# Performance work log

Hardware: AMD Instinct MI355X
Metric: run time of the kernel (lower is better)

Reference implementation:

```python
import jax, jax.numpy as jnp
import numpy as np

EPS = 1e-6
N_SRC = 100000
N_TAR = 100000
N = N_SRC + N_TAR
DIM = 128
E = 600000
NEG_SLOPE = 0.01  # torch leaky_relu default


def setup_inputs() -> dict:
    key = jax.random.key(0)
    ks = jax.random.split(key, 8)
    x_src = jax.random.normal(ks[0], (N_SRC, DIM), dtype=jnp.float32)
    x_tar = jax.random.normal(ks[1], (N_TAR, DIM), dtype=jnp.float32)
    edge_index = jax.random.randint(ks[2], (2, E), 0, N, dtype=jnp.int64)
    edge_weight = jax.random.uniform(ks[3], (E,), dtype=jnp.float32)
    W_gcn = jax.random.normal(ks[4], (DIM, DIM), dtype=jnp.float32) / np.sqrt(DIM)
    b_gcn = jax.random.normal(ks[5], (DIM,), dtype=jnp.float32) * 0.01
    W_fnn = jax.random.normal(ks[6], (DIM, DIM), dtype=jnp.float32) / np.sqrt(DIM)
    b_fnn = jax.random.normal(ks[7], (DIM,), dtype=jnp.float32) * 0.01
    return dict(x_src=x_src, x_tar=x_tar, edge_index=edge_index,
                edge_weight=edge_weight, W_gcn=W_gcn, b_gcn=b_gcn,
                W_fnn=W_fnn, b_fnn=b_fnn)


def _gcn_conv(x, edge_index, edge_weight, W, b):
    # PyG GCNConv with add_self_loops=True, symmetric normalization.
    row = jnp.concatenate([edge_index[0], jnp.arange(N, dtype=edge_index.dtype)])
    col = jnp.concatenate([edge_index[1], jnp.arange(N, dtype=edge_index.dtype)])
    w = jnp.concatenate([edge_weight, jnp.ones((N,), dtype=edge_weight.dtype)])
    deg = jax.ops.segment_sum(w, col, num_segments=N)
    dinv = jnp.where(deg > 0, jax.lax.rsqrt(deg), 0.0)
    norm = dinv[row] * w * dinv[col]                 # [E+N]
    h = x @ W                                        # [N, D]
    msg = norm[:, None] * h[row]                     # gather + scale
    out = jnp.zeros_like(h).at[col].add(msg)         # scatter-add to targets
    return out + b


def _node_norm(x):
    mean = jnp.mean(x, axis=1, keepdims=True)
    var = jnp.mean((x - mean) ** 2, axis=1, keepdims=True)  # unbiased=False
    return (x - mean) / jnp.sqrt(var + EPS)


def reference(x_src, x_tar, edge_index, edge_weight, W_gcn, b_gcn, W_fnn, b_fnn):
    x = jnp.concatenate([x_src, x_tar], axis=0)      # [N, D]
    # route == 'MIX': GNN branch + FNN branch on the skip copy
    g = _gcn_conv(x, edge_index, edge_weight, W_gcn, b_gcn)
    f = jax.nn.leaky_relu(x @ W_fnn + b_fnn, NEG_SLOPE)  # dropout = identity (eval)
    x = g + f
    x = _node_norm(x)
    x = jax.nn.leaky_relu(x, NEG_SLOPE)
    return x[:N_SRC, :], x[N_SRC:, :]
```

## Files before the change

### kernel.cpp

```cpp
#include <hip/hip_runtime.h>
#include <hip/hip_bf16.h>
#include <cstddef>
#include <cstdint>

#define DIM 128
#define SCAN_CHUNK 2048

typedef __attribute__((ext_vector_type(8))) short short8v;
typedef __attribute__((ext_vector_type(4))) float f32x4;

__device__ __forceinline__ float leaky(float v) {
    return v > 0.0f ? v : 0.01f * v;
}

__device__ __forceinline__ unsigned short f2bf(float f) {
    unsigned u = __builtin_bit_cast(unsigned, f);
    u += 0x7FFF + ((u >> 16) & 1);
    return (unsigned short)(u >> 16);
}

__device__ __forceinline__ unsigned cvt_pk_bf16(float a, float b) {
    unsigned r;
    asm("v_cvt_pk_bf16_f32 %0, %1, %2" : "=v"(r) : "v"(a), "v"(b));
    return r;
}

__device__ __forceinline__ float bf2f_hi(unsigned p) {
    return __builtin_bit_cast(float, p & 0xFFFF0000u);
}
__device__ __forceinline__ float bf2f_lo(unsigned p) {
    return __builtin_bit_cast(float, p << 16);
}

__device__ __forceinline__ void gload_lds16(const float* g, float* lds) {
    __builtin_amdgcn_global_load_lds(
        (const __attribute__((address_space(1))) unsigned int*)g,
        (__attribute__((address_space(3))) unsigned int*)lds, 16, 0, 0);
}

__global__ __launch_bounds__(256)
void hist_kernel(const int* __restrict__ col, int* __restrict__ cnt, int E,
                 const float* __restrict__ Wg, const float* __restrict__ Wf,
                 unsigned short* __restrict__ WgT, unsigned short* __restrict__ WfT) {
    int gid = blockIdx.x * blockDim.x + threadIdx.x;
    if (gid < 128 * 128) {
        int c = gid >> 7, k = gid & 127;
        WgT[c * 128 + k] = f2bf(Wg[k * 128 + c]);
        WfT[c * 128 + k] = f2bf(Wf[k * 128 + c]);
    }
    if (gid < E) atomicAdd(&cnt[col[gid]], 1);
}

__global__ __launch_bounds__(256)
void scan_block_sums(const int* __restrict__ cnt, int* __restrict__ bsum, int N) {
    __shared__ int sdata[4];
    int base = blockIdx.x * SCAN_CHUNK;
    int s = 0;
    for (int k = threadIdx.x; k < SCAN_CHUNK; k += 256) {
        int idx = base + k;
        s += (idx < N) ? cnt[idx] : 0;
    }
#pragma unroll
    for (int m = 1; m < 64; m <<= 1) s += __shfl_xor(s, m, 64);
    if ((threadIdx.x & 63) == 0) sdata[threadIdx.x >> 6] = s;
    __syncthreads();
    if (threadIdx.x == 0)
        bsum[blockIdx.x] = sdata[0] + sdata[1] + sdata[2] + sdata[3];
}

__global__ __launch_bounds__(128)
void scan_bsum_kernel(int* __restrict__ bsum, int nb) {
    __shared__ int wtot[2];
    int t = threadIdx.x;
    int lane = t & 63;
    int orig = (t < nb) ? bsum[t] : 0;
    int v = orig;
#pragma unroll
    for (int m = 1; m < 64; m <<= 1) {
        int u = __shfl_up(v, m, 64);
        if (lane >= m) v += u;
    }
    if (lane == 63) wtot[t >> 6] = v;
    __syncthreads();
    if (t >= 64) v += wtot[0];
    if (t < nb) bsum[t] = v - orig;
}

__global__ __launch_bounds__(256)
void scan_write_kernel(int* __restrict__ cnt, const int* __restrict__ bsum,
                       int* __restrict__ off, int N) {
    __shared__ int wsum[4];
    int t = threadIdx.x;
    int base = blockIdx.x * SCAN_CHUNK + t * 8;
    int vals[8];
    int local = 0;
#pragma unroll
    for (int k = 0; k < 8; ++k) {
        int idx = base + k;
        int c = (idx < N) ? cnt[idx] : 0;
        vals[k] = local;
        local += c;
    }
    int tsum = local;
    int lane = t & 63;
    int v = tsum;
#pragma unroll
    for (int m = 1; m < 64; m <<= 1) {
        int u = __shfl_up(v, m, 64);
        if (lane >= m) v += u;
    }
    if (lane == 63) wsum[t >> 6] = v;
    __syncthreads();
    int woff = 0;
    for (int i = 0; i < (t >> 6); ++i) woff += wsum[i];
    int texcl = (v - tsum) + woff + bsum[blockIdx.x];
#pragma unroll
    for (int k = 0; k < 8; ++k) {
        int idx = base + k;
        int o = texcl + vals[k];
        if (idx <= N) off[idx] = o;
    }
    __syncthreads();
#pragma unroll
    for (int k = 0; k < 8; ++k) {
        int idx = base + k;
        int o = texcl + vals[k];
        if (idx < N) cnt[idx] = o;
    }
}

__global__ __launch_bounds__(256)
void reorder_kernel(const int* __restrict__ row, const int* __restrict__ col,
                    const float* __restrict__ w, int* __restrict__ cursor,
                    int2* __restrict__ edgeRW, int E) {
    int e = blockIdx.x * blockDim.x + threadIdx.x;
    if (e < E) {
        int c = col[e];
        int pos = atomicAdd(&cursor[c], 1);
        edgeRW[pos] = make_int2(row[e], __builtin_bit_cast(int, w[e]));
    }
}

__global__ __launch_bounds__(512, 4)
void gemm_mfma_kernel(const float* __restrict__ x_src, const float* __restrict__ x_tar,
                      int n_src, int n_total, int ntiles,
                      const int* __restrict__ off, const int2* __restrict__ edgeRW,
                      const unsigned short* __restrict__ WgT,
                      const unsigned short* __restrict__ WfT,
                      const float* __restrict__ bg, const float* __restrict__ bf,
                      unsigned short* __restrict__ hsb,
                      unsigned short* __restrict__ accb)
{
    __shared__ float Ash[4][32 * 128];
    __shared__ float dinvS[448];

    const int t    = threadIdx.x;
    const int lane = t & 63;
    const int wv   = t >> 6;
    const int h    = wv >> 2;
    const int q    = wv & 3;
    const int lr   = lane & 15;
    const int lk   = lane >> 4;

    const int nb  = gridDim.x;
    const int K   = (ntiles + nb - 1) / nb;
    const int t0  = blockIdx.x * K;
    const int cnt = min(K, ntiles - t0);
    if (cnt <= 0) return;

    for (int tt = t; tt < cnt * 32; tt += 512) {
        int gi = t0 * 32 + tt;
        if (gi >= n_total) gi = n_total - 1;
        int s0 = off[gi], e0 = off[gi + 1];
        float a = 1.0f;
        for (int j = s0; j < e0; ++j)
            a += __builtin_bit_cast(float, edgeRW[j].y);
        dinvS[tt] = rsqrtf(a);
    }
    asm volatile("s_waitcnt lgkmcnt(0)" ::: "memory");
    __builtin_amdgcn_sched_barrier(0);
    asm volatile("s_waitcnt vmcnt(0)" ::: "memory");
    __builtin_amdgcn_sched_barrier(0);

    short8v wg[4][2], wf[4][2];
#pragma unroll
    for (int ks = 0; ks < 4; ++ks)
#pragma unroll
        for (int nf = 0; nf < 2; ++nf) {
            int col = q * 32 + ((lr >> 2) << 3) + nf * 4 + (lr & 3);
            const size_t bo = (size_t)col * 128 + ks * 32 + lk * 8;
            wg[ks][nf] = *(const short8v*)(WgT + bo);
            wf[ks][nf] = *(const short8v*)(WfT + bo);
        }
    const int cb = q * 32 + lk * 8;
    float4 bgv[2], bfv[2];
#pragma unroll
    for (int nf = 0; nf < 2; ++nf) {
        bgv[nf] = *(const float4*)(bg + cb + nf * 4);
        bfv[nf] = *(const float4*)(bf + cb + nf * 4);
    }
    __builtin_amdgcn_sched_barrier(0);
    asm volatile("s_waitcnt vmcnt(0)" ::: "memory");
    __builtin_amdgcn_sched_barrier(0);

    auto stage = [&](int tl, int buf) {
#pragma unroll
        for (int s = 0; s < 2; ++s) {
            int id  = s * 512 + t;
            int row = id >> 5;
            int cs  = id & 31;
            int c   = cs ^ (row & 15);
            int rg  = tl * 32 + row;
            if (rg >= n_total) rg = n_total - 1;
            const float* xr = (rg < n_src) ? x_src + (size_t)rg * DIM
                                           : x_tar + (size_t)(rg - n_src) * DIM;
            gload_lds16(xr + c * 4, &Ash[buf][(size_t)(s * 512 + wv * 64) * 4]);
        }
    };

    stage(t0, 0);
    if (1 < cnt) stage(t0 + 1, 1);
    if (2 < cnt) stage(t0 + 2, 2);

    const int xrow = h * 16 + lr;
    const int xrs  = xrow & 15;

    for (int it = 0; it < cnt; ++it) {
        if (cnt >= 6) {
            if (it == 0)              asm volatile("s_waitcnt vmcnt(4)"  ::: "memory");
            else if (it == 1)         asm volatile("s_waitcnt vmcnt(6)"  ::: "memory");
            else if (it == 2)         asm volatile("s_waitcnt vmcnt(8)"  ::: "memory");
            else if (it == cnt - 2)   asm volatile("s_waitcnt vmcnt(8)"  ::: "memory");
            else if (it == cnt - 1)   asm volatile("s_waitcnt vmcnt(6)"  ::: "memory");
            else                      asm volatile("s_waitcnt vmcnt(10)" ::: "memory");
        } else {
            asm volatile("s_waitcnt vmcnt(0)" ::: "memory");
        }
        __builtin_amdgcn_sched_barrier(0);
        __builtin_amdgcn_s_barrier();
        __builtin_amdgcn_sched_barrier(0);

        if (it + 3 < cnt) stage(t0 + it + 3, (it + 3) & 3);

        const int cur = it & 3;
        f32x4 accg[2], accf[2];
        accg[0] = (f32x4)0.0f; accg[1] = (f32x4)0.0f;
        accf[0] = (f32x4)0.0f; accf[1] = (f32x4)0.0f;

#pragma unroll
        for (int ks = 0; ks < 4; ++ks) {
            int c0 = ks * 8 + lk * 2;
            float4 q0 = *(const float4*)&Ash[cur][(size_t)(xrow * 32 + ( c0      ^ xrs)) * 4];
            float4 q1 = *(const float4*)&Ash[cur][(size_t)(xrow * 32 + ((c0 + 1) ^ xrs)) * 4];
            union { short8v v; unsigned u[4]; } cv;
            cv.u[0] = cvt_pk_bf16(q0.x, q0.y);
            cv.u[1] = cvt_pk_bf16(q0.z, q0.w);
            cv.u[2] = cvt_pk_bf16(q1.x, q1.y);
            cv.u[3] = cvt_pk_bf16(q1.z, q1.w);
#pragma unroll
            for (int nf = 0; nf < 2; ++nf) {
                accg[nf] = __builtin_amdgcn_mfma_f32_16x16x32_bf16(wg[ks][nf], cv.v, accg[nf], 0, 0, 0);
                accf[nf] = __builtin_amdgcn_mfma_f32_16x16x32_bf16(wf[ks][nf], cv.v, accf[nf], 0, 0, 0);
            }
        }

        const int tile = t0 + it;
        int r = tile * 32 + xrow;
        const bool valid = (r < n_total);
        float dv = dinvS[it * 32 + xrow];

        float hs[8], oo[8];
#pragma unroll
        for (int nf = 0; nf < 2; ++nf)
#pragma unroll
            for (int e = 0; e < 4; ++e) {
                int k = nf * 4 + e;
                hs[k] = dv * accg[nf][e];
                float f = accf[nf][e] + ((const float*)&bfv[nf])[e];
                oo[k] = leaky(f) + ((const float*)&bgv[nf])[e] + dv * hs[k];
            }

        uint4 hp, op;
        hp.x = cvt_pk_bf16(hs[0], hs[1]); hp.y = cvt_pk_bf16(hs[2], hs[3]);
        hp.z = cvt_pk_bf16(hs[4], hs[5]); hp.w = cvt_pk_bf16(hs[6], hs[7]);
        op.x = cvt_pk_bf16(oo[0], oo[1]); op.y = cvt_pk_bf16(oo[2], oo[3]);
        op.z = cvt_pk_bf16(oo[4], oo[5]); op.w = cvt_pk_bf16(oo[6], oo[7]);

        if (valid) {
            *(uint4*)(hsb  + (size_t)r * DIM + cb) = hp;
            *(uint4*)(accb + (size_t)r * DIM + cb) = op;
        }
    }
}

__global__ __launch_bounds__(256)
void gather_norm_kernel(const int* __restrict__ off, const int2* __restrict__ edgeRW,
                        const unsigned short* __restrict__ hsb,
                        const unsigned short* __restrict__ accb,
                        float* __restrict__ out, int n)
{
    const int wid  = threadIdx.x >> 6;
    const int lane = threadIdx.x & 63;
    const int sub  = lane >> 4;
    const int sl   = lane & 15;
    int i = (blockIdx.x * 4 + wid) * 4 + sub;
    if (i >= n) i = n - 1;

    const int start = off[i];
    const int degc  = off[i + 1] - start;

    int md = degc;
    md = max(md, __shfl_xor(md, 16, 64));
    md = max(md, __shfl_xor(md, 32, 64));

    float s[8];
#pragma unroll
    for (int k = 0; k < 8; ++k) s[k] = 0.0f;
    float sw = 0.0f;

    const unsigned short* gbase = hsb + (size_t)sl * 8;

    int   r0 = 0, r1 = 0;
    float w0 = 0.0f, w1 = 0.0f;
    if (0 < degc) { int2 m = edgeRW[start];     r0 = m.x; w0 = __builtin_bit_cast(float, m.y); }
    if (1 < degc) { int2 m = edgeRW[start + 1]; r1 = m.x; w1 = __builtin_bit_cast(float, m.y); }
    uint4 p0 = *(const uint4*)(gbase + (size_t)r0 * DIM);

    for (int t = 0; t < md; ++t) {
        uint4 p1 = p0;
        if (t + 1 < md)
            p1 = *(const uint4*)(gbase + (size_t)r1 * DIM);
        int r2 = 0; float w2 = 0.0f;
        if (t + 2 < md) {
            if (t + 2 < degc) {
                int2 m = edgeRW[start + t + 2];
                r2 = m.x; w2 = __builtin_bit_cast(float, m.y);
            }
        }
        sw += w0;
        s[0] += w0 * bf2f_lo(p0.x); s[1] += w0 * bf2f_hi(p0.x);
        s[2] += w0 * bf2f_lo(p0.y); s[3] += w0 * bf2f_hi(p0.y);
        s[4] += w0 * bf2f_lo(p0.z); s[5] += w0 * bf2f_hi(p0.z);
        s[6] += w0 * bf2f_lo(p0.w); s[7] += w0 * bf2f_hi(p0.w);
        p0 = p1;
        r0 = r1; w0 = w1;
        r1 = r2; w1 = w2;
    }

    const float dv = rsqrtf(1.0f + sw);
    uint4 av = *(const uint4*)(accb + (size_t)i * DIM + sl * 8);
    float v[8];
    v[0] = bf2f_lo(av.x) + dv * s[0]; v[1] = bf2f_hi(av.x) + dv * s[1];
    v[2] = bf2f_lo(av.y) + dv * s[2]; v[3] = bf2f_hi(av.y) + dv * s[3];
    v[4] = bf2f_lo(av.z) + dv * s[4]; v[5] = bf2f_hi(av.z) + dv * s[5];
    v[6] = bf2f_lo(av.w) + dv * s[6]; v[7] = bf2f_hi(av.w) + dv * s[7];

    float sum = 0.0f;
#pragma unroll
    for (int k = 0; k < 8; ++k) sum += v[k];
#pragma unroll
    for (int m = 1; m < 16; m <<= 1) sum += __shfl_xor(sum, m, 64);
    const float mean = sum * (1.0f / 128.0f);

    float sq = 0.0f;
#pragma unroll
    for (int k = 0; k < 8; ++k) {
        v[k] -= mean;
        sq += v[k] * v[k];
    }
#pragma unroll
    for (int m = 1; m < 16; m <<= 1) sq += __shfl_xor(sq, m, 64);
    const float rstd = rsqrtf(sq * (1.0f / 128.0f) + 1e-6f);

    float4 o1, o2;
    o1.x = leaky(v[0] * rstd); o1.y = leaky(v[1] * rstd);
    o1.z = leaky(v[2] * rstd); o1.w = leaky(v[3] * rstd);
    o2.x = leaky(v[4] * rstd); o2.y = leaky(v[5] * rstd);
    o2.z = leaky(v[6] * rstd); o2.w = leaky(v[7] * rstd);
    float* op = out + (size_t)i * DIM + sl * 8;
    *(float4*)op       = o1;
    *(float4*)(op + 4) = o2;
}

extern "C" void kernel_launch(void* const* d_in, const int* in_sizes, int n_in,
                              void* d_out, int out_size, void* d_ws, size_t ws_size,
                              hipStream_t stream)
{
    const float* x_src = (const float*)d_in[0];
    const float* x_tar = (const float*)d_in[1];
    const int*   ei    = (const int*)d_in[2];
    const float* ew    = (const float*)d_in[3];
    const float* Wg    = (const float*)d_in[4];
    const float* bg    = (const float*)d_in[5];
    const float* Wf    = (const float*)d_in[6];
    const float* bf    = (const float*)d_in[7];

    const int n_src = in_sizes[0] / DIM;
    const int n_tar = in_sizes[1] / DIM;
    const int N     = n_src + n_tar;
    const int E     = in_sizes[3];

    const int* rowp = ei;
    const int* colp = ei + E;

    char* p = (char*)d_ws;
    int*   cnt  = (int*)p;    p += (size_t)N * 4;
    int*   off  = (int*)p;    p += (size_t)(N + 1) * 4;
    int*   bsum = (int*)p;    p += 160 * 4;
    p = (char*)(((uintptr_t)p + 15) & ~(uintptr_t)15);
    int2*  edgeRW = (int2*)p; p += (size_t)E * 8;
    unsigned short* hsb  = (unsigned short*)p; p += (size_t)N * DIM * 2;
    unsigned short* accb = (unsigned short*)p; p += (size_t)N * DIM * 2;
    unsigned short* WgT  = (unsigned short*)p; p += 128 * 128 * 2;
    unsigned short* WfT  = (unsigned short*)p;

    const int NB = (N + 1 + SCAN_CHUNK - 1) / SCAN_CHUNK;

    hipMemsetAsync(cnt, 0, (size_t)N * sizeof(int), stream);

    hist_kernel<<<(E + 255) / 256, 256, 0, stream>>>(colp, cnt, E,
                                                     Wg, Wf, WgT, WfT);

    scan_block_sums<<<NB, 256, 0, stream>>>(cnt, bsum, N);
    scan_bsum_kernel<<<1, 128, 0, stream>>>(bsum, NB);
    scan_write_kernel<<<NB, 256, 0, stream>>>(cnt, bsum, off, N);

    reorder_kernel<<<(E + 255) / 256, 256, 0, stream>>>(rowp, colp, ew, cnt,
                                                        edgeRW, E);

    const int ntiles = (N + 31) / 32;
    gemm_mfma_kernel<<<512, 512, 0, stream>>>(
        x_src, x_tar, n_src, N, ntiles, off, edgeRW, WgT, WfT, bg, bf,
        hsb, accb);

    gather_norm_kernel<<<(N + 15) / 16, 256, 0, stream>>>(
        off, edgeRW, hsb, accb, (float*)d_out, N);
}
```

Baseline: 190.4 us.

## Fuse CSR build stages into one cooperative kernel with grid syncs

Replaces the memset, histogram, three scan kernels and reorder kernel with a single cooperative kernel that uses grid-wide barriers between phases. It removes several kernel launches and their inter-kernel gaps. In exchange the work runs on a fixed 512-block grid with grid-stride loops, and each grid.sync adds barrier latency. NB must be at most 512 and at most 128 for the scan to be correct; it is about 98 here.

```diff
diff --git a/kernel.cpp b/kernel.cpp
--- a/kernel.cpp
+++ b/kernel.cpp
@@ -1,7 +1,10 @@
 #include <hip/hip_runtime.h>
 #include <hip/hip_bf16.h>
+#include <hip/hip_cooperative_groups.h>
 #include <cstddef>
 #include <cstdint>
+
+namespace cg = cooperative_groups;
 
 #define DIM 128
 #define SCAN_CHUNK 2048
@@ -39,105 +42,110 @@
 }
 
 __global__ __launch_bounds__(256)
-void hist_kernel(const int* __restrict__ col, int* __restrict__ cnt, int E,
-                 const float* __restrict__ Wg, const float* __restrict__ Wf,
-                 unsigned short* __restrict__ WgT, unsigned short* __restrict__ WfT) {
-    int gid = blockIdx.x * blockDim.x + threadIdx.x;
-    if (gid < 128 * 128) {
-        int c = gid >> 7, k = gid & 127;
+void build_csr_kernel(const int* __restrict__ rowp, const int* __restrict__ colp,
+                      const float* __restrict__ ew, int E,
+                      const float* __restrict__ Wg, const float* __restrict__ Wf,
+                      unsigned short* __restrict__ WgT, unsigned short* __restrict__ WfT,
+                      int* __restrict__ cnt, int* __restrict__ off,
+                      int* __restrict__ bsum, int2* __restrict__ edgeRW,
+                      int N, int NB)
+{
+    cg::grid_group grid = cg::this_grid();
+    const int gid = blockIdx.x * 256 + threadIdx.x;
+    const int gsz = gridDim.x * 256;
+
+    for (int t = gid; t < N; t += gsz) cnt[t] = 0;
+    for (int t = gid; t < 128 * 128; t += gsz) {
+        int c = t >> 7, k = t & 127;
         WgT[c * 128 + k] = f2bf(Wg[k * 128 + c]);
         WfT[c * 128 + k] = f2bf(Wf[k * 128 + c]);
     }
-    if (gid < E) atomicAdd(&cnt[col[gid]], 1);
-}
-
-__global__ __launch_bounds__(256)
-void scan_block_sums(const int* __restrict__ cnt, int* __restrict__ bsum, int N) {
+    grid.sync();
+
+    for (int e = gid; e < E; e += gsz) atomicAdd(&cnt[colp[e]], 1);
+    grid.sync();
+
     __shared__ int sdata[4];
-    int base = blockIdx.x * SCAN_CHUNK;
-    int s = 0;
-    for (int k = threadIdx.x; k < SCAN_CHUNK; k += 256) {
-        int idx = base + k;
-        s += (idx < N) ? cnt[idx] : 0;
-    }
-#pragma unroll
-    for (int m = 1; m < 64; m <<= 1) s += __shfl_xor(s, m, 64);
-    if ((threadIdx.x & 63) == 0) sdata[threadIdx.x >> 6] = s;
-    __syncthreads();
-    if (threadIdx.x == 0)
-        bsum[blockIdx.x] = sdata[0] + sdata[1] + sdata[2] + sdata[3];
-}
-
-__global__ __launch_bounds__(128)
-void scan_bsum_kernel(int* __restrict__ bsum, int nb) {
-    __shared__ int wtot[2];
-    int t = threadIdx.x;
-    int lane = t & 63;
-    int orig = (t < nb) ? bsum[t] : 0;
-    int v = orig;
-#pragma unroll
-    for (int m = 1; m < 64; m <<= 1) {
-        int u = __shfl_up(v, m, 64);
-        if (lane >= m) v += u;
-    }
-    if (lane == 63) wtot[t >> 6] = v;
-    __syncthreads();
-    if (t >= 64) v += wtot[0];
-    if (t < nb) bsum[t] = v - orig;
-}
-
-__global__ __launch_bounds__(256)
-void scan_write_kernel(int* __restrict__ cnt, const int* __restrict__ bsum,
-                       int* __restrict__ off, int N) {
+    if (blockIdx.x < NB) {
+        int base = blockIdx.x * SCAN_CHUNK;
+        int s = 0;
+        for (int k = threadIdx.x; k < SCAN_CHUNK; k += 256) {
+            int idx = base + k;
+            s += (idx < N) ? cnt[idx] : 0;
+        }
+#pragma unroll
+        for (int m = 1; m < 64; m <<= 1) s += __shfl_xor(s, m, 64);
+        if ((threadIdx.x & 63) == 0) sdata[threadIdx.x >> 6] = s;
+        __syncthreads();
+        if (threadIdx.x == 0)
+            bsum[blockIdx.x] = sdata[0] + sdata[1] + sdata[2] + sdata[3];
+    }
+    grid.sync();
+
+    if (blockIdx.x == 0) {
+        __shared__ int wtot[2];
+        int t = threadIdx.x;
+        int lane = t & 63;
+        int orig = (t < 128 && t < NB) ? bsum[t] : 0;
+        int v = orig;
+#pragma unroll
+        for (int m = 1; m < 64; m <<= 1) {
+            int u = __shfl_up(v, m, 64);
+            if (lane >= m) v += u;
+        }
+        if (t < 128 && lane == 63) wtot[t >> 6] = v;
+        __syncthreads();
+        if (t >= 64 && t < 128) v += wtot[0];
+        if (t < 128 && t < NB) bsum[t] = v - orig;
+    }
+    grid.sync();
+
     __shared__ int wsum[4];
-    int t = threadIdx.x;
-    int base = blockIdx.x * SCAN_CHUNK + t * 8;
-    int vals[8];
-    int local = 0;
-#pragma unroll
-    for (int k = 0; k < 8; ++k) {
-        int idx = base + k;
-        int c = (idx < N) ? cnt[idx] : 0;
-        vals[k] = local;
-        local += c;
-    }
-    int tsum = local;
-    int lane = t & 63;
-    int v = tsum;
-#pragma unroll
-    for (int m = 1; m < 64; m <<= 1) {
-        int u = __shfl_up(v, m, 64);
-        if (lane >= m) v += u;
-    }
-    if (lane == 63) wsum[t >> 6] = v;
-    __syncthreads();
-    int woff = 0;
-    for (int i = 0; i < (t >> 6); ++i) woff += wsum[i];
-    int texcl = (v - tsum) + woff + bsum[blockIdx.x];
-#pragma unroll
-    for (int k = 0; k < 8; ++k) {
-        int idx = base + k;
-        int o = texcl + vals[k];
-        if (idx <= N) off[idx] = o;
-    }
-    __syncthreads();
-#pragma unroll
-    for (int k = 0; k < 8; ++k) {
-        int idx = base + k;
-        int o = texcl + vals[k];
-        if (idx < N) cnt[idx] = o;
-    }
-}
-
-__global__ __launch_bounds__(256)
-void reorder_kernel(const int* __restrict__ row, const int* __restrict__ col,
-                    const float* __restrict__ w, int* __restrict__ cursor,
-                    int2* __restrict__ edgeRW, int E) {
-    int e = blockIdx.x * blockDim.x + threadIdx.x;
-    if (e < E) {
-        int c = col[e];
-        int pos = atomicAdd(&cursor[c], 1);
-        edgeRW[pos] = make_int2(row[e], __builtin_bit_cast(int, w[e]));
+    if (blockIdx.x < NB) {
+        int t = threadIdx.x;
+        int base = blockIdx.x * SCAN_CHUNK + t * 8;
+        int vals[8];
+        int local = 0;
+#pragma unroll
+        for (int k = 0; k < 8; ++k) {
+            int idx = base + k;
+            int c = (idx < N) ? cnt[idx] : 0;
+            vals[k] = local;
+            local += c;
+        }
+        int tsum = local;
+        int lane = t & 63;
+        int v = tsum;
+#pragma unroll
+        for (int m = 1; m < 64; m <<= 1) {
+            int u = __shfl_up(v, m, 64);
+            if (lane >= m) v += u;
+        }
+        if (lane == 63) wsum[t >> 6] = v;
+        __syncthreads();
+        int woff = 0;
+        for (int i = 0; i < (t >> 6); ++i) woff += wsum[i];
+        int texcl = (v - tsum) + woff + bsum[blockIdx.x];
+#pragma unroll
+        for (int k = 0; k < 8; ++k) {
+            int idx = base + k;
+            int o = texcl + vals[k];
+            if (idx <= N) off[idx] = o;
+        }
+        __syncthreads();
+#pragma unroll
+        for (int k = 0; k < 8; ++k) {
+            int idx = base + k;
+            int o = texcl + vals[k];
+            if (idx < N) cnt[idx] = o;
+        }
+    }
+    grid.sync();
+
+    for (int e = gid; e < E; e += gsz) {
+        int c = colp[e];
+        int pos = atomicAdd(&cnt[c], 1);
+        edgeRW[pos] = make_int2(rowp[e], __builtin_bit_cast(int, ew[e]));
     }
 }
 
@@ -416,17 +424,27 @@
 
     const int NB = (N + 1 + SCAN_CHUNK - 1) / SCAN_CHUNK;
 
-    hipMemsetAsync(cnt, 0, (size_t)N * sizeof(int), stream);
-
-    hist_kernel<<<(E + 255) / 256, 256, 0, stream>>>(colp, cnt, E,
-                                                     Wg, Wf, WgT, WfT);
-
-    scan_block_sums<<<NB, 256, 0, stream>>>(cnt, bsum, N);
-    scan_bsum_kernel<<<1, 128, 0, stream>>>(bsum, NB);
-    scan_write_kernel<<<NB, 256, 0, stream>>>(cnt, bsum, off, N);
-
-    reorder_kernel<<<(E + 255) / 256, 256, 0, stream>>>(rowp, colp, ew, cnt,
-                                                        edgeRW, E);
+    {
+        const int*   a_rowp = rowp;
+        const int*   a_colp = colp;
+        const float* a_ew   = ew;
+        int          a_E    = E;
+        const float* a_Wg   = Wg;
+        const float* a_Wf   = Wf;
+        unsigned short* a_WgT = WgT;
+        unsigned short* a_WfT = WfT;
+        int*  a_cnt  = cnt;
+        int*  a_off  = off;
+        int*  a_bsum = bsum;
+        int2* a_edge = edgeRW;
+        int   a_N    = N;
+        int   a_NB   = NB;
+        void* args[] = { &a_rowp, &a_colp, &a_ew, &a_E, &a_Wg, &a_Wf,
+                         &a_WgT, &a_WfT, &a_cnt, &a_off, &a_bsum, &a_edge,
+                         &a_N, &a_NB };
+        hipLaunchCooperativeKernel((const void*)build_csr_kernel,
+                                   dim3(512), dim3(256), args, 0, stream);
+    }
 
     const int ntiles = (N + 31) / 32;
     gemm_mfma_kernel<<<512, 512, 0, stream>>>(
```

Result: slower. 451.3 us (+137.0%).
